# Performance work log

Hardware: AMD Instinct MI355X
Metric: run time of the kernel (lower is better)

## Reference

```python
import jax, jax.numpy as jnp
import numpy as np

N_NODES = 50000
N_EDGES = 800000
D_IN = 128
HIDDEN = 128
N_CLASSES = 40


def _sage_conv(x, edge_index, W_l, b_l, W_r, num_nodes):
    # PyG SAGEConv (aggr='mean'): out = lin_l(mean_j x_src_j) + lin_r(x_dst)
    src, dst = edge_index[0], edge_index[1]
    msg = x[src]                                              # [E, D] gather
    agg = jax.ops.segment_sum(msg, dst, num_segments=num_nodes)
    deg = jax.ops.segment_sum(jnp.ones((edge_index.shape[1],), x.dtype), dst,
                              num_segments=num_nodes)
    agg = agg / jnp.maximum(deg, 1.0)[:, None]                # scatter-mean
    return agg @ W_l + b_l + x @ W_r


def setup_inputs() -> dict:
    key = jax.random.key(0)
    k1, k2, k3, k4, k5, k6, k7 = jax.random.split(key, 7)
    s1 = 1.0 / np.sqrt(D_IN)
    s2 = 1.0 / np.sqrt(HIDDEN)
    return {
        "x": jax.random.normal(k1, (N_NODES, D_IN), dtype=jnp.float32),
        "edge_index": jax.random.randint(k2, (2, N_EDGES), 0, N_NODES, dtype=jnp.int64),
        "W1_l": jax.random.uniform(k3, (D_IN, HIDDEN), jnp.float32, -s1, s1),
        "b1": jnp.zeros((HIDDEN,), jnp.float32),
        "W1_r": jax.random.uniform(k4, (D_IN, HIDDEN), jnp.float32, -s1, s1),
        "W2_l": jax.random.uniform(k5, (HIDDEN, N_CLASSES), jnp.float32, -s2, s2),
        "b2": jnp.zeros((N_CLASSES,), jnp.float32),
        "W2_r": jax.random.uniform(k6, (HIDDEN, N_CLASSES), jnp.float32, -s2, s2),
    }


def reference(x, edge_index, W1_l, b1, W1_r, W2_l, b2, W2_r):
    # eval mode: F.dropout(training=False) is identity
    h = _sage_conv(x, edge_index, W1_l, b1, W1_r, N_NODES)
    h = jax.nn.relu(h)
    out = _sage_conv(h, edge_index, W2_l, b2, W2_r, N_NODES)
    return out
```

## Files before the change

### kernel.cpp

```cpp
#include <hip/hip_runtime.h>
#include <hip/hip_fp8.h>

#define N_NODES 50000
#define N_EDGES 800000
#define D_IN 128
#define HIDDEN 128
#define N_CLASSES 40

#define M_PAD 50048
#define CAP 64
#define EDGE_BATCH_BLOCKS 391

typedef __attribute__((ext_vector_type(8))) short short8;
typedef __attribute__((ext_vector_type(4))) float floatx4;

static __device__ __forceinline__ unsigned short f2bf(float f) {
    unsigned u = __float_as_uint(f);
    u = (u + 0x7fffu + ((u >> 16) & 1u)) >> 16;
    return (unsigned short)u;
}
static __device__ __forceinline__ float bf2f(unsigned short b) {
    return __uint_as_float(((unsigned)b) << 16);
}
static __device__ __forceinline__ unsigned char f2fp8(float v) {
    __hip_fp8_e4m3 t(v);
    return (unsigned char)t.__x;
}
static __device__ __forceinline__ float fp82f(unsigned char b) {
    __hip_fp8_e4m3 t;
    t.__x = (__hip_fp8_storage_t)b;
    return (float)t;
}

#define KP_W1 128
#define KP_W2 40
#define KP_CNT 196
#define KP_GRID (KP_W1 + KP_W2 + KP_CNT)

__global__ __launch_bounds__(256) void prep_kernel(
    const float* __restrict__ W1l, const float* __restrict__ W1r,
    unsigned short* __restrict__ Wt1, const float* __restrict__ W2l,
    const float* __restrict__ W2r, unsigned short* __restrict__ Wt2,
    int* __restrict__ cnt) {
    int b = blockIdx.x;
    int t = threadIdx.x;
    if (b < KP_W1) {
        int i = b * 256 + t;
        int n = i >> 7, k = i & 127;
        float v = (n < 128) ? W1l[k * 128 + n] : W1r[k * 128 + (n - 128)];
        Wt1[n * 128 + k] = f2bf(v);
    } else if (b < KP_W1 + KP_W2) {
        int i = (b - KP_W1) * 256 + t;
        int n = i >> 7, k = i & 127;
        float v = (n < 40) ? W2l[k * 40 + n] : W2r[k * 40 + (n - 40)];
        Wt2[n * 128 + k] = f2bf(v);
    } else {
        int i = (b - KP_W1 - KP_W2) * 256 + t;
        if (i < N_NODES) cnt[i] = 0;
    }
}

__global__ __launch_bounds__(256) void fill_bucket_kernel(
    const int* __restrict__ src, const int* __restrict__ dst,
    int* __restrict__ cnt, unsigned short* __restrict__ bucket) {
    int i0 = (blockIdx.x * 256 + threadIdx.x) * 8;
    if (i0 >= N_EDGES) return;
    int4 d0 = *(const int4*)(dst + i0);
    int4 d1 = *(const int4*)(dst + i0 + 4);
    int4 s0 = *(const int4*)(src + i0);
    int4 s1 = *(const int4*)(src + i0 + 4);
    int p0 = atomicAdd(&cnt[d0.x], 1);
    int p1 = atomicAdd(&cnt[d0.y], 1);
    int p2 = atomicAdd(&cnt[d0.z], 1);
    int p3 = atomicAdd(&cnt[d0.w], 1);
    int p4 = atomicAdd(&cnt[d1.x], 1);
    int p5 = atomicAdd(&cnt[d1.y], 1);
    int p6 = atomicAdd(&cnt[d1.z], 1);
    int p7 = atomicAdd(&cnt[d1.w], 1);
    if (p0 < CAP) bucket[d0.x * CAP + p0] = (unsigned short)s0.x;
    if (p1 < CAP) bucket[d0.y * CAP + p1] = (unsigned short)s0.y;
    if (p2 < CAP) bucket[d0.z * CAP + p2] = (unsigned short)s0.z;
    if (p3 < CAP) bucket[d0.w * CAP + p3] = (unsigned short)s0.w;
    if (p4 < CAP) bucket[d1.x * CAP + p4] = (unsigned short)s1.x;
    if (p5 < CAP) bucket[d1.y * CAP + p5] = (unsigned short)s1.y;
    if (p6 < CAP) bucket[d1.z * CAP + p6] = (unsigned short)s1.z;
    if (p7 < CAP) bucket[d1.w * CAP + p7] = (unsigned short)s1.w;
}

#define A_LD 136

__global__ __launch_bounds__(256) void gemm1_mfma_kernel(
    const float* __restrict__ x, const unsigned short* __restrict__ Wt,
    unsigned char* __restrict__ ylb, unsigned short* __restrict__ yrb) {
    __shared__ unsigned short sA[64][A_LD];

    const int wave = threadIdx.x >> 6;
    const int lane = threadIdx.x & 63;
    const int r = lane & 15, q = lane >> 4;
    const int m0 = blockIdx.x * 64;
    const int n0 = wave * 64;
    const int t = threadIdx.x;

#pragma unroll
    for (int i = 0; i < 8; i++) {
        int g = t + i * 256;
        int row = g >> 5;
        int k4 = (g & 31) << 2;
        int gr = m0 + row;
        if (gr >= N_NODES) gr = N_NODES - 1;
        float4 v = *(const float4*)(x + (size_t)gr * 128 + k4);
        uint2 p;
        p.x = (unsigned)f2bf(v.x) | ((unsigned)f2bf(v.y) << 16);
        p.y = (unsigned)f2bf(v.z) | ((unsigned)f2bf(v.w) << 16);
        *(uint2*)&sA[row][k4] = p;
    }
    __syncthreads();

    floatx4 acc[4][4];
#pragma unroll
    for (int i = 0; i < 4; i++)
#pragma unroll
        for (int j = 0; j < 4; j++) acc[i][j] = (floatx4){0.f, 0.f, 0.f, 0.f};

#pragma unroll
    for (int kc = 0; kc < 128; kc += 32) {
        short8 a[4], bb[4];
#pragma unroll
        for (int mi = 0; mi < 4; mi++)
            a[mi] = *(const short8*)&sA[mi * 16 + r][kc + q * 8];
#pragma unroll
        for (int ni = 0; ni < 4; ni++)
            bb[ni] = *(const short8*)(Wt + (size_t)(n0 + ni * 16 + r) * 128 + kc + q * 8);
#pragma unroll
        for (int mi = 0; mi < 4; mi++)
#pragma unroll
            for (int ni = 0; ni < 4; ni++)
                acc[mi][ni] = __builtin_amdgcn_mfma_f32_16x16x32_bf16(
                    a[mi], bb[ni], acc[mi][ni], 0, 0, 0);
    }

#pragma unroll
    for (int mi = 0; mi < 4; mi++) {
        int rowb = m0 + mi * 16 + q * 4;
#pragma unroll
        for (int ni = 0; ni < 4; ni++) {
            int col = n0 + ni * 16 + r;
#pragma unroll
            for (int reg = 0; reg < 4; reg++) {
                int gr = rowb + reg;
                if (gr < N_NODES) {
                    float v = acc[mi][ni][reg];
                    if (col < 128)
                        ylb[(size_t)gr * 128 + col] = f2fp8(v);
                    else
                        yrb[(size_t)gr * 128 + (col - 128)] = f2bf(v);
                }
            }
        }
    }
}

__global__ __launch_bounds__(256) void gemm2_mfma_kernel(
    const unsigned short* __restrict__ hb, const unsigned short* __restrict__ Wt,
    unsigned short* __restrict__ zlb, unsigned short* __restrict__ zrb) {
    const int wave = threadIdx.x >> 6;
    const int lane = threadIdx.x & 63;
    const int r = lane & 15, q = lane >> 4;
    const int m0 = blockIdx.x * 64 + wave * 16;

    floatx4 acc[5];
#pragma unroll
    for (int i = 0; i < 5; i++) acc[i] = (floatx4){0.f, 0.f, 0.f, 0.f};

#pragma unroll
    for (int kc = 0; kc < 128; kc += 32) {
        short8 a = *(const short8*)(hb + (size_t)(m0 + r) * 128 + kc + q * 8);
        short8 b[5];
#pragma unroll
        for (int ni = 0; ni < 5; ni++)
            b[ni] = *(const short8*)(Wt + (size_t)(ni * 16 + r) * 128 + kc + q * 8);
#pragma unroll
        for (int ni = 0; ni < 5; ni++)
            acc[ni] = __builtin_amdgcn_mfma_f32_16x16x32_bf16(a, b[ni], acc[ni], 0, 0, 0);
    }

    int rowb = m0 + q * 4;
#pragma unroll
    for (int ni = 0; ni < 5; ni++) {
        int col = ni * 16 + r;
#pragma unroll
        for (int reg = 0; reg < 4; reg++) {
            int gr = rowb + reg;
            if (gr < N_NODES) {
                unsigned short v = f2bf(acc[ni][reg]);
                if (col < 40)
                    zlb[(size_t)gr * 40 + col] = v;
                else
                    zrb[(size_t)gr * 40 + (col - 40)] = v;
            }
        }
    }
}

__global__ __launch_bounds__(256) void agg_relu1_kernel(
    const unsigned short* __restrict__ yl8, const int* __restrict__ cnt,
    const unsigned short* __restrict__ bucket, const float2* __restrict__ b12,
    const unsigned int* __restrict__ yru, unsigned int* __restrict__ hbu) {
    int n = blockIdx.x * 4 + (threadIdx.x >> 6);
    if (n >= N_NODES) return;
    int l = threadIdx.x & 63;
    int deg = cnt[n];
    int re = min(deg, CAP);
    const unsigned short* bk = bucket + n * CAP;
    float ax = 0.f, ay = 0.f, bx = 0.f, by = 0.f;
    int e = 0;
    for (; e + 7 < re; e += 8) {
        unsigned short u[8];
#pragma unroll
        for (int j = 0; j < 8; j++) {
            int s = bk[e + j];
            u[j] = yl8[(size_t)s * 64 + l];
        }
#pragma unroll
        for (int j = 0; j < 8; j += 2) {
            ax += fp82f(u[j] & 0xff); ay += fp82f(u[j] >> 8);
            bx += fp82f(u[j + 1] & 0xff); by += fp82f(u[j + 1] >> 8);
        }
    }
    for (; e + 3 < re; e += 4) {
        int s0 = bk[e + 0], s1 = bk[e + 1], s2 = bk[e + 2], s3 = bk[e + 3];
        unsigned short u0 = yl8[(size_t)s0 * 64 + l];
        unsigned short u1 = yl8[(size_t)s1 * 64 + l];
        unsigned short u2 = yl8[(size_t)s2 * 64 + l];
        unsigned short u3 = yl8[(size_t)s3 * 64 + l];
        ax += fp82f(u0 & 0xff); ay += fp82f(u0 >> 8);
        bx += fp82f(u1 & 0xff); by += fp82f(u1 >> 8);
        ax += fp82f(u2 & 0xff); ay += fp82f(u2 >> 8);
        bx += fp82f(u3 & 0xff); by += fp82f(u3 >> 8);
    }
    for (; e < re; e++) {
        unsigned short u0 = yl8[(size_t)bk[e] * 64 + l];
        ax += fp82f(u0 & 0xff); ay += fp82f(u0 >> 8);
    }
    float inv = 1.0f / (float)max(deg, 1);
    unsigned ur = yru[(size_t)n * 64 + l];
    float2 b = b12[l];
    float ox = fmaxf((ax + bx) * inv + bf2f(ur & 0xffff) + b.x, 0.0f);
    float oy = fmaxf((ay + by) * inv + bf2f(ur >> 16) + b.y, 0.0f);
    hbu[(size_t)n * 64 + l] = (unsigned)f2bf(ox) | ((unsigned)f2bf(oy) << 16);
}

__global__ __launch_bounds__(256) void agg_out2_kernel(
    const unsigned short* __restrict__ zlb, const unsigned short* __restrict__ zrb,
    const int* __restrict__ cnt, const unsigned short* __restrict__ bucket,
    const float* __restrict__ b2, float* __restrict__ out) {
    int n = blockIdx.x * 4 + (threadIdx.x >> 6);
    if (n >= N_NODES) return;
    int c = threadIdx.x & 63;
    if (c >= N_CLASSES) return;
    int deg = cnt[n];
    int re = min(deg, CAP);
    const unsigned short* bk = bucket + n * CAP;
    float a0 = 0.f, a1 = 0.f;
    int e = 0;
    for (; e + 3 < re; e += 4) {
        int s0 = bk[e + 0], s1 = bk[e + 1], s2 = bk[e + 2], s3 = bk[e + 3];
        float v0 = bf2f(zlb[(size_t)s0 * 40 + c]);
        float v1 = bf2f(zlb[(size_t)s1 * 40 + c]);
        float v2 = bf2f(zlb[(size_t)s2 * 40 + c]);
        float v3 = bf2f(zlb[(size_t)s3 * 40 + c]);
        a0 += v0 + v2;
        a1 += v1 + v3;
    }
    for (; e < re; e++) a0 += bf2f(zlb[(size_t)bk[e] * 40 + c]);
    float inv = 1.0f / (float)max(deg, 1);
    out[(size_t)n * 40 + c] =
        (a0 + a1) * inv + bf2f(zrb[(size_t)n * 40 + c]) + b2[c];
}

extern "C" void kernel_launch(void* const* d_in, const int* in_sizes, int n_in,
                              void* d_out, int out_size, void* d_ws, size_t ws_size,
                              hipStream_t stream) {
    const float* x   = (const float*)d_in[0];
    const int*   ei  = (const int*)d_in[1];
    const float* W1l = (const float*)d_in[2];
    const float* b1  = (const float*)d_in[3];
    const float* W1r = (const float*)d_in[4];
    const float* W2l = (const float*)d_in[5];
    const float* b2  = (const float*)d_in[6];
    const float* W2r = (const float*)d_in[7];
    float* out = (float*)d_out;

    const int* src = ei;
    const int* dst = ei + N_EDGES;

    char* ws = (char*)d_ws;
    int* cnt               = (int*)(ws);
    unsigned short* bucket = (unsigned short*)(ws + 262144);
    unsigned short* Wt1    = (unsigned short*)(ws + 6662144);
    unsigned short* Wt2    = (unsigned short*)(ws + 6727680);
    unsigned short* hb     = (unsigned short*)(ws + 6748160);
    unsigned char*  ylb    = (unsigned char*)(ws + 19560448);
    unsigned short* yrb    = (unsigned short*)(ws + 25960448);
    unsigned short* zlb    = (unsigned short*)(ws + 38760448);
    unsigned short* zrb    = (unsigned short*)(ws + 42760448);

    prep_kernel<<<KP_GRID, 256, 0, stream>>>(W1l, W1r, Wt1, W2l, W2r, Wt2, cnt);
    fill_bucket_kernel<<<EDGE_BATCH_BLOCKS, 256, 0, stream>>>(src, dst, cnt,
                                                              bucket);

    const int AGG_BLOCKS = (N_NODES + 3) / 4;

    gemm1_mfma_kernel<<<M_PAD / 64, 256, 0, stream>>>(x, Wt1, ylb, yrb);
    agg_relu1_kernel<<<AGG_BLOCKS, 256, 0, stream>>>(
        (const unsigned short*)ylb, cnt, bucket, (const float2*)b1,
        (const unsigned int*)yrb, (unsigned int*)hb);

    gemm2_mfma_kernel<<<M_PAD / 64, 256, 0, stream>>>(hb, Wt2, zlb, zrb);
    agg_out2_kernel<<<AGG_BLOCKS, 256, 0, stream>>>(
        zlb, zrb, cnt, bucket, b2, out);
}
```

Before: 218.7 us.

## Fuse layer-1 aggregation with layer-2 GEMM through shared memory

Merges the layer-1 mean aggregation plus ReLU kernel with the layer-2 MFMA GEMM. Each block aggregates 64 nodes into a bf16 tile in LDS, then runs the GEMM directly from LDS. This removes the global write and read of the hidden activation buffer and one kernel launch. In exchange, each block is 16x larger and processes 16 nodes per wave sequentially, so there are far fewer blocks (782 vs 12500) to hide gather latency. The MFMA stage also waits on a block-wide sync, which may lower parallelism.

```diff
diff --git a/kernel.cpp b/kernel.cpp
--- a/kernel.cpp
+++ b/kernel.cpp
@@ -160,13 +160,69 @@
     }
 }
 
-__global__ __launch_bounds__(256) void gemm2_mfma_kernel(
-    const unsigned short* __restrict__ hb, const unsigned short* __restrict__ Wt,
+__global__ __launch_bounds__(256) void agg1_gemm2_kernel(
+    const unsigned short* __restrict__ yl8, const int* __restrict__ cnt,
+    const unsigned short* __restrict__ bucket, const float2* __restrict__ b12,
+    const unsigned int* __restrict__ yru, const unsigned short* __restrict__ Wt,
     unsigned short* __restrict__ zlb, unsigned short* __restrict__ zrb) {
+    __shared__ unsigned short sH[64][A_LD];
+
     const int wave = threadIdx.x >> 6;
     const int lane = threadIdx.x & 63;
+    const int m0 = blockIdx.x * 64;
+
+    float2 b = b12[lane];
+#pragma unroll 1
+    for (int i = 0; i < 16; i++) {
+        int row = wave + i * 4;
+        int n = m0 + row;
+        float ox = 0.f, oy = 0.f;
+        if (n < N_NODES) {
+            int deg = cnt[n];
+            int re = min(deg, CAP);
+            const unsigned short* bk = bucket + n * CAP;
+            float ax = 0.f, ay = 0.f, bx = 0.f, by = 0.f;
+            int e = 0;
+            for (; e + 7 < re; e += 8) {
+                unsigned short u[8];
+#pragma unroll
+                for (int j = 0; j < 8; j++) {
+                    int s = bk[e + j];
+                    u[j] = yl8[(size_t)s * 64 + lane];
+                }
+#pragma unroll
+                for (int j = 0; j < 8; j += 2) {
+                    ax += fp82f(u[j] & 0xff); ay += fp82f(u[j] >> 8);
+                    bx += fp82f(u[j + 1] & 0xff); by += fp82f(u[j + 1] >> 8);
+                }
+            }
+            for (; e + 3 < re; e += 4) {
+                int s0 = bk[e + 0], s1 = bk[e + 1], s2 = bk[e + 2], s3 = bk[e + 3];
+                unsigned short u0 = yl8[(size_t)s0 * 64 + lane];
+                unsigned short u1 = yl8[(size_t)s1 * 64 + lane];
+                unsigned short u2 = yl8[(size_t)s2 * 64 + lane];
+                unsigned short u3 = yl8[(size_t)s3 * 64 + lane];
+                ax += fp82f(u0 & 0xff); ay += fp82f(u0 >> 8);
+                bx += fp82f(u1 & 0xff); by += fp82f(u1 >> 8);
+                ax += fp82f(u2 & 0xff); ay += fp82f(u2 >> 8);
+                bx += fp82f(u3 & 0xff); by += fp82f(u3 >> 8);
+            }
+            for (; e < re; e++) {
+                unsigned short u0 = yl8[(size_t)bk[e] * 64 + lane];
+                ax += fp82f(u0 & 0xff); ay += fp82f(u0 >> 8);
+            }
+            float inv = 1.0f / (float)max(deg, 1);
+            unsigned ur = yru[(size_t)n * 64 + lane];
+            ox = fmaxf((ax + bx) * inv + bf2f(ur & 0xffff) + b.x, 0.0f);
+            oy = fmaxf((ay + by) * inv + bf2f(ur >> 16) + b.y, 0.0f);
+        }
+        unsigned pk = (unsigned)f2bf(ox) | ((unsigned)f2bf(oy) << 16);
+        *(unsigned*)&sH[row][2 * lane] = pk;
+    }
+    __syncthreads();
+
     const int r = lane & 15, q = lane >> 4;
-    const int m0 = blockIdx.x * 64 + wave * 16;
+    const int rl = wave * 16;
 
     floatx4 acc[5];
 #pragma unroll
@@ -174,17 +230,17 @@
 
 #pragma unroll
     for (int kc = 0; kc < 128; kc += 32) {
-        short8 a = *(const short8*)(hb + (size_t)(m0 + r) * 128 + kc + q * 8);
-        short8 b[5];
+        short8 a = *(const short8*)&sH[rl + r][kc + q * 8];
+        short8 bb[5];
 #pragma unroll
         for (int ni = 0; ni < 5; ni++)
-            b[ni] = *(const short8*)(Wt + (size_t)(ni * 16 + r) * 128 + kc + q * 8);
+            bb[ni] = *(const short8*)(Wt + (size_t)(ni * 16 + r) * 128 + kc + q * 8);
 #pragma unroll
         for (int ni = 0; ni < 5; ni++)
-            acc[ni] = __builtin_amdgcn_mfma_f32_16x16x32_bf16(a, b[ni], acc[ni], 0, 0, 0);
-    }
-
-    int rowb = m0 + q * 4;
+            acc[ni] = __builtin_amdgcn_mfma_f32_16x16x32_bf16(a, bb[ni], acc[ni], 0, 0, 0);
+    }
+
+    int rowb = m0 + rl + q * 4;
 #pragma unroll
     for (int ni = 0; ni < 5; ni++) {
         int col = ni * 16 + r;
@@ -200,54 +256,6 @@
             }
         }
     }
-}
-
-__global__ __launch_bounds__(256) void agg_relu1_kernel(
-    const unsigned short* __restrict__ yl8, const int* __restrict__ cnt,
-    const unsigned short* __restrict__ bucket, const float2* __restrict__ b12,
-    const unsigned int* __restrict__ yru, unsigned int* __restrict__ hbu) {
-    int n = blockIdx.x * 4 + (threadIdx.x >> 6);
-    if (n >= N_NODES) return;
-    int l = threadIdx.x & 63;
-    int deg = cnt[n];
-    int re = min(deg, CAP);
-    const unsigned short* bk = bucket + n * CAP;
-    float ax = 0.f, ay = 0.f, bx = 0.f, by = 0.f;
-    int e = 0;
-    for (; e + 7 < re; e += 8) {
-        unsigned short u[8];
-#pragma unroll
-        for (int j = 0; j < 8; j++) {
-            int s = bk[e + j];
-            u[j] = yl8[(size_t)s * 64 + l];
-        }
-#pragma unroll
-        for (int j = 0; j < 8; j += 2) {
-            ax += fp82f(u[j] & 0xff); ay += fp82f(u[j] >> 8);
-            bx += fp82f(u[j + 1] & 0xff); by += fp82f(u[j + 1] >> 8);
-        }
-    }
-    for (; e + 3 < re; e += 4) {
-        int s0 = bk[e + 0], s1 = bk[e + 1], s2 = bk[e + 2], s3 = bk[e + 3];
-        unsigned short u0 = yl8[(size_t)s0 * 64 + l];
-        unsigned short u1 = yl8[(size_t)s1 * 64 + l];
-        unsigned short u2 = yl8[(size_t)s2 * 64 + l];
-        unsigned short u3 = yl8[(size_t)s3 * 64 + l];
-        ax += fp82f(u0 & 0xff); ay += fp82f(u0 >> 8);
-        bx += fp82f(u1 & 0xff); by += fp82f(u1 >> 8);
-        ax += fp82f(u2 & 0xff); ay += fp82f(u2 >> 8);
-        bx += fp82f(u3 & 0xff); by += fp82f(u3 >> 8);
-    }
-    for (; e < re; e++) {
-        unsigned short u0 = yl8[(size_t)bk[e] * 64 + l];
-        ax += fp82f(u0 & 0xff); ay += fp82f(u0 >> 8);
-    }
-    float inv = 1.0f / (float)max(deg, 1);
-    unsigned ur = yru[(size_t)n * 64 + l];
-    float2 b = b12[l];
-    float ox = fmaxf((ax + bx) * inv + bf2f(ur & 0xffff) + b.x, 0.0f);
-    float oy = fmaxf((ay + by) * inv + bf2f(ur >> 16) + b.y, 0.0f);
-    hbu[(size_t)n * 64 + l] = (unsigned)f2bf(ox) | ((unsigned)f2bf(oy) << 16);
 }
 
 __global__ __launch_bounds__(256) void agg_out2_kernel(
@@ -299,24 +307,21 @@
     unsigned short* bucket = (unsigned short*)(ws + 262144);
     unsigned short* Wt1    = (unsigned short*)(ws + 6662144);
     unsigned short* Wt2    = (unsigned short*)(ws + 6727680);
-    unsigned short* hb     = (unsigned short*)(ws + 6748160);
-    unsigned char*  ylb    = (unsigned char*)(ws + 19560448);
-    unsigned short* yrb    = (unsigned short*)(ws + 25960448);
-    unsigned short* zlb    = (unsigned short*)(ws + 38760448);
-    unsigned short* zrb    = (unsigned short*)(ws + 42760448);
+    unsigned char*  ylb    = (unsigned char*)(ws + 6748160);
+    unsigned short* yrb    = (unsigned short*)(ws + 13148160);
+    unsigned short* zlb    = (unsigned short*)(ws + 25948160);
+    unsigned short* zrb    = (unsigned short*)(ws + 29948160);
 
     prep_kernel<<<KP_GRID, 256, 0, stream>>>(W1l, W1r, Wt1, W2l, W2r, Wt2, cnt);
     fill_bucket_kernel<<<EDGE_BATCH_BLOCKS, 256, 0, stream>>>(src, dst, cnt,
                                                               bucket);
 
-    const int AGG_BLOCKS = (N_NODES + 3) / 4;
-
     gemm1_mfma_kernel<<<M_PAD / 64, 256, 0, stream>>>(x, Wt1, ylb, yrb);
-    agg_relu1_kernel<<<AGG_BLOCKS, 256, 0, stream>>>(
+
+    agg1_gemm2_kernel<<<M_PAD / 64, 256, 0, stream>>>(
         (const unsigned short*)ylb, cnt, bucket, (const float2*)b1,
-        (const unsigned int*)yrb, (unsigned int*)hb);
-
-    gemm2_mfma_kernel<<<M_PAD / 64, 256, 0, stream>>>(hb, Wt2, zlb, zrb);
-    agg_out2_kernel<<<AGG_BLOCKS, 256, 0, stream>>>(
+        (const unsigned int*)yrb, Wt2, zlb, zrb);
+
+    agg_out2_kernel<<<(N_NODES + 3) / 4, 256, 0, stream>>>(
         zlb, zrb, cnt, bucket, b2, out);
 }
```

New measurement: 238.1 us. 1.09x slower.

## Split gemm1 across a 2D grid and load A directly without LDS

Applied to the files above, without the earlier changes.

The first GEMM kernel no longer stages the bf16-converted x tile in shared memory. Each wave now owns 16 rows and reads x straight from global memory, converting to bf16 in registers. A second grid dimension splits the 256 output columns into the fp8 left half and the bf16 right half. This removes the LDS staging and barrier, doubles the number of blocks, and cuts per-thread accumulators from 16 to 8, which may help occupancy. The cost is that x is read twice, once per column half, and each wave reuses its A operand less.

```diff
diff --git a/kernel.cpp b/kernel.cpp
--- a/kernel.cpp
+++ b/kernel.cpp
@@ -87,74 +87,61 @@
     if (p7 < CAP) bucket[d1.w * CAP + p7] = (unsigned short)s1.w;
 }
 
-#define A_LD 136
-
 __global__ __launch_bounds__(256) void gemm1_mfma_kernel(
     const float* __restrict__ x, const unsigned short* __restrict__ Wt,
     unsigned char* __restrict__ ylb, unsigned short* __restrict__ yrb) {
-    __shared__ unsigned short sA[64][A_LD];
-
     const int wave = threadIdx.x >> 6;
     const int lane = threadIdx.x & 63;
     const int r = lane & 15, q = lane >> 4;
-    const int m0 = blockIdx.x * 64;
-    const int n0 = wave * 64;
-    const int t = threadIdx.x;
-
-#pragma unroll
-    for (int i = 0; i < 8; i++) {
-        int g = t + i * 256;
-        int row = g >> 5;
-        int k4 = (g & 31) << 2;
-        int gr = m0 + row;
-        if (gr >= N_NODES) gr = N_NODES - 1;
-        float4 v = *(const float4*)(x + (size_t)gr * 128 + k4);
-        uint2 p;
-        p.x = (unsigned)f2bf(v.x) | ((unsigned)f2bf(v.y) << 16);
-        p.y = (unsigned)f2bf(v.z) | ((unsigned)f2bf(v.w) << 16);
-        *(uint2*)&sA[row][k4] = p;
-    }
-    __syncthreads();
-
-    floatx4 acc[4][4];
-#pragma unroll
-    for (int i = 0; i < 4; i++)
-#pragma unroll
-        for (int j = 0; j < 4; j++) acc[i][j] = (floatx4){0.f, 0.f, 0.f, 0.f};
+    const int m0 = blockIdx.x * 64 + wave * 16;
+    const int nbase = blockIdx.y * 128;
+
+    floatx4 acc[8];
+#pragma unroll
+    for (int i = 0; i < 8; i++) acc[i] = (floatx4){0.f, 0.f, 0.f, 0.f};
+
+    int gr_a = m0 + r;
+    if (gr_a >= N_NODES) gr_a = N_NODES - 1;
+    const float* xrow = x + (size_t)gr_a * 128;
 
 #pragma unroll
     for (int kc = 0; kc < 128; kc += 32) {
-        short8 a[4], bb[4];
-#pragma unroll
-        for (int mi = 0; mi < 4; mi++)
-            a[mi] = *(const short8*)&sA[mi * 16 + r][kc + q * 8];
-#pragma unroll
-        for (int ni = 0; ni < 4; ni++)
-            bb[ni] = *(const short8*)(Wt + (size_t)(n0 + ni * 16 + r) * 128 + kc + q * 8);
-#pragma unroll
-        for (int mi = 0; mi < 4; mi++)
-#pragma unroll
-            for (int ni = 0; ni < 4; ni++)
-                acc[mi][ni] = __builtin_amdgcn_mfma_f32_16x16x32_bf16(
-                    a[mi], bb[ni], acc[mi][ni], 0, 0, 0);
-    }
-
-#pragma unroll
-    for (int mi = 0; mi < 4; mi++) {
-        int rowb = m0 + mi * 16 + q * 4;
-#pragma unroll
-        for (int ni = 0; ni < 4; ni++) {
-            int col = n0 + ni * 16 + r;
+        float4 v0 = *(const float4*)(xrow + kc + q * 8);
+        float4 v1 = *(const float4*)(xrow + kc + q * 8 + 4);
+        uint4 u;
+        u.x = (unsigned)f2bf(v0.x) | ((unsigned)f2bf(v0.y) << 16);
+        u.y = (unsigned)f2bf(v0.z) | ((unsigned)f2bf(v0.w) << 16);
+        u.z = (unsigned)f2bf(v1.x) | ((unsigned)f2bf(v1.y) << 16);
+        u.w = (unsigned)f2bf(v1.z) | ((unsigned)f2bf(v1.w) << 16);
+        short8 a = *(short8*)&u;
+        short8 b[8];
+#pragma unroll
+        for (int ni = 0; ni < 8; ni++)
+            b[ni] = *(const short8*)(Wt + (size_t)(nbase + ni * 16 + r) * 128 + kc + q * 8);
+#pragma unroll
+        for (int ni = 0; ni < 8; ni++)
+            acc[ni] = __builtin_amdgcn_mfma_f32_16x16x32_bf16(a, b[ni], acc[ni], 0, 0, 0);
+    }
+
+    int rowb = m0 + q * 4;
+    if (blockIdx.y == 0) {
+#pragma unroll
+        for (int ni = 0; ni < 8; ni++) {
+            int col = ni * 16 + r;
 #pragma unroll
             for (int reg = 0; reg < 4; reg++) {
                 int gr = rowb + reg;
-                if (gr < N_NODES) {
-                    float v = acc[mi][ni][reg];
-                    if (col < 128)
-                        ylb[(size_t)gr * 128 + col] = f2fp8(v);
-                    else
-                        yrb[(size_t)gr * 128 + (col - 128)] = f2bf(v);
-                }
+                if (gr < N_NODES) ylb[(size_t)gr * 128 + col] = f2fp8(acc[ni][reg]);
+            }
+        }
+    } else {
+#pragma unroll
+        for (int ni = 0; ni < 8; ni++) {
+            int col = ni * 16 + r;
+#pragma unroll
+            for (int reg = 0; reg < 4; reg++) {
+                int gr = rowb + reg;
+                if (gr < N_NODES) yrb[(size_t)gr * 128 + col] = f2bf(acc[ni][reg]);
             }
         }
     }
@@ -311,7 +298,10 @@
 
     const int AGG_BLOCKS = (N_NODES + 3) / 4;
 
-    gemm1_mfma_kernel<<<M_PAD / 64, 256, 0, stream>>>(x, Wt1, ylb, yrb);
+    {
+        dim3 grid(M_PAD / 64, 2);
+        gemm1_mfma_kernel<<<grid, 256, 0, stream>>>(x, Wt1, ylb, yrb);
+    }
     agg_relu1_kernel<<<AGG_BLOCKS, 256, 0, stream>>>(
         (const unsigned short*)ylb, cnt, bucket, (const float2*)b1,
         (const unsigned int*)yrb, (unsigned int*)hb);
```

Result: slower. 233.9 us, median of 2 (+6.9%).
